# Kernel optimization log

Measured on AMD Instinct MI355X. Metric: run time of the kernel, lower is better.

## Reference

```python
import jax, jax.numpy as jnp
import numpy as np

K = 2  # forward hardcodes k = 2, overriding the k_vector argmax


def setup_inputs() -> dict:
    key = jax.random.key(0)
    k1, k2, k3 = jax.random.split(key, 3)
    points = jax.random.uniform(k1, (4, 8000, 3), dtype=jnp.float32)
    preds = jax.random.uniform(k2, (4, 8000, 256), dtype=jnp.float32)
    k_vector = jax.random.normal(k3, (2,), dtype=jnp.float32)
    return {"points": points, "preds": preds, "k_vector": k_vector}


def reference(points, preds, k_vector):
    # k = argmax(softmax(k_vector)) + 1 is computed then discarded; k = 2.
    # Pairwise euclidean distance (torch.cdist, p=2): [B, N, N]
    sq = jnp.sum(points * points, axis=-1)  # [B, N]
    d2 = sq[:, :, None] + sq[:, None, :] - 2.0 * jnp.einsum(
        'bnd,bmd->bnm', points, points)
    dist = jnp.sqrt(jnp.maximum(d2, 0.0))
    # k smallest distances -> indices of K nearest neighbors (incl. self)
    _, idx = jax.lax.top_k(-dist, K)  # idx: [B, N, K]
    # Gather neighbor features and average: [B, N, K, C] -> [B, N, C]
    knn_preds = jax.vmap(lambda p, i: p[i])(preds, idx)
    return jnp.mean(knn_preds, axis=2)
```

## Files before the change

### kernel.cpp

```cpp
#include <hip/hip_runtime.h>
#include <math.h>

#define BATCH 4
#define NPTS  8000
#define NCH   256
#define GDIM  20
#define NCELL (GDIM*GDIM*GDIM)
#define CELLH (1.0f/GDIM)
#define EPS   1e-5f

#define STRIDE_ST (NCELL + 16)
#define WS_STARTS 0
#define WS_PSORT  131072

__device__ __forceinline__ int cell_clamp(float v) {
  int c = (int)(v * (float)GDIM);
  return c < 0 ? 0 : (c > GDIM - 1 ? GDIM - 1 : c);
}

__global__ __launch_bounds__(1024) void build_kernel(const float* __restrict__ points,
                                                     int* __restrict__ starts,
                                                     float4* __restrict__ psort) {
  __shared__ int lst[NCELL];
  __shared__ int wtot[16];
  const int t = threadIdx.x;
  const int b = blockIdx.x;
  if (t < 1000) {
#pragma unroll
    for (int k = 0; k < 8; ++k) lst[t * 8 + k] = 0;
  }
  __syncthreads();

  const float* pb = points + (size_t)b * NPTS * 3;
  float px[8], py[8], pz[8];
  int pc[8];
  if (t < 1000) {
    const float4* pv = (const float4*)pb;
    const float4 a0 = pv[t * 6 + 0], a1 = pv[t * 6 + 1], a2 = pv[t * 6 + 2];
    const float4 a3 = pv[t * 6 + 3], a4 = pv[t * 6 + 4], a5 = pv[t * 6 + 5];
    px[0] = a0.x; py[0] = a0.y; pz[0] = a0.z;
    px[1] = a0.w; py[1] = a1.x; pz[1] = a1.y;
    px[2] = a1.z; py[2] = a1.w; pz[2] = a2.x;
    px[3] = a2.y; py[3] = a2.z; pz[3] = a2.w;
    px[4] = a3.x; py[4] = a3.y; pz[4] = a3.z;
    px[5] = a3.w; py[5] = a4.x; pz[5] = a4.y;
    px[6] = a4.z; py[6] = a4.w; pz[6] = a5.x;
    px[7] = a5.y; py[7] = a5.z; pz[7] = a5.w;
#pragma unroll
    for (int k = 0; k < 8; ++k) {
      pc[k] = (cell_clamp(pz[k]) * GDIM + cell_clamp(py[k])) * GDIM + cell_clamp(px[k]);
      atomicAdd(&lst[pc[k]], 1);
    }
  }
  __syncthreads();

  int v[8];
  int sum = 0;
  if (t < 1000) {
#pragma unroll
    for (int k = 0; k < 8; ++k) {
      v[k] = lst[t * 8 + k];
      sum += v[k];
    }
  }
  const int lane = t & 63, wv = t >> 6;
  int incl = sum;
#pragma unroll
  for (int d = 1; d < 64; d <<= 1) {
    const int u = __shfl_up(incl, d);
    if (lane >= d) incl += u;
  }
  if (lane == 63) wtot[wv] = incl;
  __syncthreads();
  if (wv == 0) {
    int x = (lane < 16) ? wtot[lane] : 0;
#pragma unroll
    for (int d = 1; d < 16; d <<= 1) {
      const int u = __shfl_up(x, d);
      if (lane >= d) x += u;
    }
    if (lane < 16) wtot[lane] = x;
  }
  __syncthreads();
  const int base = incl - sum + (wv ? wtot[wv - 1] : 0);

  int* stg = starts + b * STRIDE_ST;
  if (t < 1000) {
    int run = base;
#pragma unroll
    for (int k = 0; k < 8; ++k) {
      stg[t * 8 + k] = run;
      lst[t * 8 + k] = run;
      run += v[k];
    }
  }
  if (t == 0) stg[NCELL] = NPTS;
  __syncthreads();

  float4* psb = psort + (size_t)b * NPTS;
  if (t < 1000) {
#pragma unroll
    for (int k = 0; k < 8; ++k) {
      const int pos = atomicAdd(&lst[pc[k]], 1);
      psb[pos] = make_float4(px[k], py[k], pz[k], __int_as_float(t * 8 + k));
    }
  }
}

#define SCAN_RANGE(P0, P1)                                        \
  for (int p = (P0); p < (P1); ++p) {                             \
    const float4 P = ps[p];                                       \
    const float dot = xi * P.x + yi * P.y + zi * P.z;             \
    const float sqj = P.x * P.x + P.y * P.y + P.z * P.z;          \
    const float d2 = fmaxf((sqi + sqj) - 2.0f * dot, 0.0f);       \
    const int j = __float_as_int(P.w);                            \
    const bool lt = (p != i) &&                                   \
        ((d2 < b0) || (d2 == b0 && j < j0));                      \
    b0 = lt ? d2 : b0;                                            \
    j0 = lt ? j : j0;                                             \
  }

#define MERGE_XOR(MASK)                                           \
  {                                                               \
    const float ob = __shfl_xor(mb0, MASK);                       \
    const int oj = __shfl_xor(mj0, MASK);                         \
    const bool keep = (mb0 < ob) || (mb0 == ob && mj0 < oj);      \
    mb0 = keep ? mb0 : ob;                                        \
    mj0 = keep ? mj0 : oj;                                        \
  }

__global__ __launch_bounds__(256, 8) void search_gather_kernel(
    const float4* __restrict__ psort, const int* __restrict__ starts,
    const float* __restrict__ preds, float* __restrict__ out) {
  const int t = threadIdx.x;
  const int b = blockIdx.y;
  const int ql = t >> 4;
  const int s = t & 15;
  const int i = blockIdx.x * 16 + ql;
  const int* stg = starts + b * STRIDE_ST;
  const float4* ps = psort + (size_t)b * NPTS;
  const float4 Q = ps[i];
  const float xi = Q.x, yi = Q.y, zi = Q.z;
  const int qorig = __float_as_int(Q.w);
  const float sqi = xi * xi + yi * yi + zi * zi;
  const int cx = cell_clamp(xi), cy = cell_clamp(yi), cz = cell_clamp(zi);

  float b0 = INFINITY;
  int j0 = -1;

  {
    int lo0 = 0, hi0 = 0, lo1 = 0, hi1 = 0;
    {
      const int c = s;
      const int dz = c / 9 - 1;
      const int rem = c % 9;
      const int z = cz + dz, y = cy + rem / 3 - 1, x = cx + rem % 3 - 1;
      if ((unsigned)z < GDIM && (unsigned)y < GDIM && (unsigned)x < GDIM) {
        const int cid = (z * GDIM + y) * GDIM + x;
        lo0 = stg[cid];
        hi0 = stg[cid + 1];
      }
    }
    if (s < 11) {
      const int c = s + 16;
      const int dz = c / 9 - 1;
      const int rem = c % 9;
      const int z = cz + dz, y = cy + rem / 3 - 1, x = cx + rem % 3 - 1;
      if ((unsigned)z < GDIM && (unsigned)y < GDIM && (unsigned)x < GDIM) {
        const int cid = (z * GDIM + y) * GDIM + x;
        lo1 = stg[cid];
        hi1 = stg[cid + 1];
      }
    }
    SCAN_RANGE(lo0, hi0)
    SCAN_RANGE(lo1, hi1)
  }

  float mb0 = b0;
  int mj0 = j0;
  MERGE_XOR(1) MERGE_XOR(2) MERGE_XOR(4) MERGE_XOR(8)

  if (!(mb0 + EPS <= CELLH * CELLH)) {
    const int x0c = cx > 1 ? cx - 2 : 0;
    const int x1c = cx < GDIM - 2 ? cx + 2 : GDIM - 1;
    int rs[2], re[2];
#pragma unroll
    for (int rr = 0; rr < 2; ++rr) {
      const int kk = s + rr * 16;
      int lo = 0, hi = 0;
      if (kk < 25) {
        const int z = cz + kk / 5 - 2;
        const int y = cy + kk % 5 - 2;
        if ((unsigned)z < GDIM && (unsigned)y < GDIM) {
          const int rowbase = (z * GDIM + y) * GDIM;
          lo = stg[rowbase + x0c];
          hi = stg[rowbase + x1c + 1];
        }
      }
      rs[rr] = lo;
      re[rr] = hi;
    }
#pragma unroll
    for (int rr = 0; rr < 2; ++rr) { SCAN_RANGE(rs[rr], re[rr]) }

    mb0 = b0; mj0 = j0;
    MERGE_XOR(1) MERGE_XOR(2) MERGE_XOR(4) MERGE_XOR(8)

    if (!(mb0 + EPS <= (2.0f * CELLH) * (2.0f * CELLH))) {
      for (int r = 3; r <= GDIM; ++r) {
        const int W = 2 * r + 1;
        for (int idx = s; idx < W * W; idx += 16) {
          const int dz = idx / W - r;
          const int dy = idx % W - r;
          const int z = cz + dz, y = cy + dy;
          if ((unsigned)z >= GDIM || (unsigned)y >= GDIM) continue;
          const int rowbase = (z * GDIM + y) * GDIM;
          if (dz == -r || dz == r || dy == -r || dy == r) {
            const int xl = cx > r ? cx - r : 0;
            const int xh = cx < GDIM - 1 - r ? cx + r : GDIM - 1;
            const int lo = stg[rowbase + xl], hi = stg[rowbase + xh + 1];
            SCAN_RANGE(lo, hi)
          } else {
            if (cx - r >= 0) {
              const int lo = stg[rowbase + cx - r], hi = stg[rowbase + cx - r + 1];
              SCAN_RANGE(lo, hi)
            }
            if (cx + r <= GDIM - 1) {
              const int lo = stg[rowbase + cx + r], hi = stg[rowbase + cx + r + 1];
              SCAN_RANGE(lo, hi)
            }
          }
        }
        mb0 = b0; mj0 = j0;
        MERGE_XOR(1) MERGE_XOR(2) MERGE_XOR(4) MERGE_XOR(8)
        const float rb = (float)r * CELLH;
        if (mb0 + EPS <= rb * rb) break;
      }
    }
  }

  const int lane = t & 63;
  const float* predb = preds + (size_t)b * NPTS * NCH;
  float* outb = out + (size_t)b * NPTS * NCH;
#pragma unroll
  for (int k = 0; k < 4; ++k) {
    const int c = __shfl(mj0, k * 16);
    const int qo = __shfl(qorig, k * 16);
    const float4 va = ((const float4*)(predb + (size_t)qo * NCH))[lane];
    const float4 vc = ((const float4*)(predb + (size_t)c * NCH))[lane];
    float4 r;
    r.x = 0.5f * (va.x + vc.x);
    r.y = 0.5f * (va.y + vc.y);
    r.z = 0.5f * (va.z + vc.z);
    r.w = 0.5f * (va.w + vc.w);
    ((float4*)(outb + (size_t)qo * NCH))[lane] = r;
  }
}

extern "C" void kernel_launch(void* const* d_in, const int* in_sizes, int n_in,
                              void* d_out, int out_size, void* d_ws, size_t ws_size,
                              hipStream_t stream) {
  const float* points = (const float*)d_in[0];
  const float* preds = (const float*)d_in[1];
  float* out = (float*)d_out;

  char* ws = (char*)d_ws;
  int* starts = (int*)(ws + WS_STARTS);
  float4* psort = (float4*)(ws + WS_PSORT);

  build_kernel<<<BATCH, 1024, 0, stream>>>(points, starts, psort);
  search_gather_kernel<<<dim3(NPTS / 16, BATCH), 256, 0, stream>>>(psort, starts, preds, out);
}
```

Baseline: 34.58 us.

## Replace sorted-grid build with fixed-capacity atomic cell buckets plus spill list

Adds a new path that zeroes per-cell counters, then bins every point in parallel into fixed 5-slot cell buckets with atomics. Points that overflow a bucket go to a per-batch spill list that every query scans. This replaces the earlier build, which ran only one 1024-thread block per batch to do a count/scan/scatter, with a grid-wide build meant to remove that serial latency. Queries now run in original point order. The spill list is capped at 512 entries per batch, and points beyond that cap would be dropped silently; the path is used only when the workspace is large enough.

```diff
diff --git a/kernel.cpp b/kernel.cpp
--- a/kernel.cpp
+++ b/kernel.cpp
@@ -9,14 +9,199 @@
 #define CELLH (1.0f/GDIM)
 #define EPS   1e-5f
 
+#define CAPN  5
+#define SPCAP 512
+#define WS2_CNT   0
+#define WS2_SPILL 131072
+#define WS2_PTS   163840
+#define WS2_TOTAL (163840 + (size_t)BATCH * NCELL * CAPN * 16)
+
 #define STRIDE_ST (NCELL + 16)
 #define WS_STARTS 0
 #define WS_PSORT  131072
+#define WS_FB_TOTAL 643072
 
 __device__ __forceinline__ int cell_clamp(float v) {
   int c = (int)(v * (float)GDIM);
   return c < 0 ? 0 : (c > GDIM - 1 ? GDIM - 1 : c);
 }
+
+
+__global__ void zero_cnt_kernel(int* __restrict__ cnt) {
+  const int g = blockIdx.x * 256 + threadIdx.x;
+  if (g < BATCH * NCELL + BATCH) cnt[g] = 0;
+}
+
+__global__ void build_cap_kernel(const float* __restrict__ points,
+                                 int* __restrict__ cnt,
+                                 float4* __restrict__ cell_pts,
+                                 float4* __restrict__ spill) {
+  const int g = blockIdx.x * 256 + threadIdx.x;
+  if (g >= BATCH * NPTS) return;
+  const int b = g / NPTS;
+  const int j = g - b * NPTS;
+  const float* p = points + (size_t)b * NPTS * 3 + (size_t)j * 3;
+  const float x = p[0], y = p[1], z = p[2];
+  const int cid = (cell_clamp(z) * GDIM + cell_clamp(y)) * GDIM + cell_clamp(x);
+  const float4 rec = make_float4(x, y, z, __int_as_float(j));
+  const int pos = atomicAdd(&cnt[b * NCELL + cid], 1);
+  if (pos < CAPN) {
+    cell_pts[((size_t)b * NCELL + cid) * CAPN + pos] = rec;
+  } else {
+    int* spc = cnt + BATCH * NCELL;
+    const int sp = atomicAdd(&spc[b], 1);
+    if (sp < SPCAP) spill[b * SPCAP + sp] = rec;
+  }
+}
+
+#define CAP_CAND(P)                                               \
+  {                                                               \
+    const float dot = xi * (P).x + yi * (P).y + zi * (P).z;       \
+    const float sqj = (P).x * (P).x + (P).y * (P).y + (P).z * (P).z; \
+    const float d2 = fmaxf((sqi + sqj) - 2.0f * dot, 0.0f);       \
+    const int j = __float_as_int((P).w);                          \
+    const bool lt = (j != i) &&                                   \
+        ((d2 < b0) || (d2 == b0 && j < j0));                      \
+    b0 = lt ? d2 : b0;                                            \
+    j0 = lt ? j : j0;                                             \
+  }
+
+#define CAP_SCAN_CELL(CID)                                        \
+  {                                                               \
+    int n = cntb[(CID)];                                          \
+    n = n < CAPN ? n : CAPN;                                      \
+    const float4* base = cpb + (size_t)(CID) * CAPN;              \
+    for (int slot = 0; slot < n; ++slot) {                        \
+      const float4 P = base[slot];                                \
+      CAP_CAND(P)                                                 \
+    }                                                             \
+  }
+
+#define MERGE_XOR(MASK)                                           \
+  {                                                               \
+    const float ob = __shfl_xor(mb0, MASK);                       \
+    const int oj = __shfl_xor(mj0, MASK);                         \
+    const bool keep = (mb0 < ob) || (mb0 == ob && mj0 < oj);      \
+    mb0 = keep ? mb0 : ob;                                        \
+    mj0 = keep ? mj0 : oj;                                        \
+  }
+
+__global__ __launch_bounds__(256, 8) void search_gather_cap_kernel(
+    const float* __restrict__ points, const int* __restrict__ cnt,
+    const float4* __restrict__ cell_pts, const float4* __restrict__ spill,
+    const float* __restrict__ preds, float* __restrict__ out) {
+  const int t = threadIdx.x;
+  const int b = blockIdx.y;
+  const int ql = t >> 4;
+  const int s = t & 15;
+  const int i = blockIdx.x * 16 + ql;
+  const float* pb = points + (size_t)b * NPTS * 3;
+  const float xi = pb[i * 3 + 0];
+  const float yi = pb[i * 3 + 1];
+  const float zi = pb[i * 3 + 2];
+  const float sqi = xi * xi + yi * yi + zi * zi;
+  const int cx = cell_clamp(xi), cy = cell_clamp(yi), cz = cell_clamp(zi);
+  const int* cntb = cnt + b * NCELL;
+  const float4* cpb = cell_pts + (size_t)b * NCELL * CAPN;
+
+  float b0 = INFINITY;
+  int j0 = -1;
+
+  {
+    const int c = s;
+    const int dz = c / 9 - 1;
+    const int rem = c % 9;
+    const int z = cz + dz, y = cy + rem / 3 - 1, x = cx + rem % 3 - 1;
+    if ((unsigned)z < GDIM && (unsigned)y < GDIM && (unsigned)x < GDIM) {
+      const int cid = (z * GDIM + y) * GDIM + x;
+      CAP_SCAN_CELL(cid)
+    }
+  }
+  if (s < 11) {
+    const int c = s + 16;
+    const int dz = c / 9 - 1;
+    const int rem = c % 9;
+    const int z = cz + dz, y = cy + rem / 3 - 1, x = cx + rem % 3 - 1;
+    if ((unsigned)z < GDIM && (unsigned)y < GDIM && (unsigned)x < GDIM) {
+      const int cid = (z * GDIM + y) * GDIM + x;
+      CAP_SCAN_CELL(cid)
+    }
+  }
+  {
+    const int spn = cnt[BATCH * NCELL + b];
+    const float4* spb = spill + b * SPCAP;
+    for (int u = s; u < spn; u += 16) {
+      const float4 P = spb[u];
+      CAP_CAND(P)
+    }
+  }
+
+  float mb0 = b0;
+  int mj0 = j0;
+  MERGE_XOR(1) MERGE_XOR(2) MERGE_XOR(4) MERGE_XOR(8)
+
+  if (!(mb0 + EPS <= CELLH * CELLH)) {
+#pragma unroll
+    for (int k = 0; k < 8; ++k) {
+      const int c = s + k * 16;
+      if (c < 125) {
+        const int dz = c / 25 - 2;
+        const int rem = c % 25;
+        const int z = cz + dz, y = cy + rem / 5 - 2, x = cx + rem % 5 - 2;
+        if ((unsigned)z < GDIM && (unsigned)y < GDIM && (unsigned)x < GDIM) {
+          const int cid = (z * GDIM + y) * GDIM + x;
+          CAP_SCAN_CELL(cid)
+        }
+      }
+    }
+    mb0 = b0; mj0 = j0;
+    MERGE_XOR(1) MERGE_XOR(2) MERGE_XOR(4) MERGE_XOR(8)
+
+    if (!(mb0 + EPS <= (2.0f * CELLH) * (2.0f * CELLH))) {
+      for (int r = 3; r <= GDIM; ++r) {
+        const int W = 2 * r + 1;
+        for (int idx = s; idx < W * W; idx += 16) {
+          const int dz = idx / W - r;
+          const int dy = idx % W - r;
+          const int z = cz + dz, y = cy + dy;
+          if ((unsigned)z >= GDIM || (unsigned)y >= GDIM) continue;
+          const int rowbase = (z * GDIM + y) * GDIM;
+          if (dz == -r || dz == r || dy == -r || dy == r) {
+            const int xl = cx > r ? cx - r : 0;
+            const int xh = cx < GDIM - 1 - r ? cx + r : GDIM - 1;
+            for (int x = xl; x <= xh; ++x) CAP_SCAN_CELL(rowbase + x)
+          } else {
+            if (cx - r >= 0) CAP_SCAN_CELL(rowbase + cx - r)
+            if (cx + r <= GDIM - 1) CAP_SCAN_CELL(rowbase + cx + r)
+          }
+        }
+        mb0 = b0; mj0 = j0;
+        MERGE_XOR(1) MERGE_XOR(2) MERGE_XOR(4) MERGE_XOR(8)
+        const float rb = (float)r * CELLH;
+        if (mb0 + EPS <= rb * rb) break;
+      }
+    }
+  }
+
+  const int wv = t >> 6;
+  const int lane = t & 63;
+  const float* predb = preds + (size_t)b * NPTS * NCH;
+  float* outb = out + (size_t)b * NPTS * NCH;
+#pragma unroll
+  for (int k = 0; k < 4; ++k) {
+    const int c = __shfl(mj0, k * 16);
+    const int qo = blockIdx.x * 16 + wv * 4 + k;
+    const float4 va = ((const float4*)(predb + (size_t)qo * NCH))[lane];
+    const float4 vc = ((const float4*)(predb + (size_t)c * NCH))[lane];
+    float4 r;
+    r.x = 0.5f * (va.x + vc.x);
+    r.y = 0.5f * (va.y + vc.y);
+    r.z = 0.5f * (va.z + vc.z);
+    r.w = 0.5f * (va.w + vc.w);
+    ((float4*)(outb + (size_t)qo * NCH))[lane] = r;
+  }
+}
+
 
 __global__ __launch_bounds__(1024) void build_kernel(const float* __restrict__ points,
                                                      int* __restrict__ starts,
@@ -118,15 +303,6 @@
         ((d2 < b0) || (d2 == b0 && j < j0));                      \
     b0 = lt ? d2 : b0;                                            \
     j0 = lt ? j : j0;                                             \
-  }
-
-#define MERGE_XOR(MASK)                                           \
-  {                                                               \
-    const float ob = __shfl_xor(mb0, MASK);                       \
-    const int oj = __shfl_xor(mj0, MASK);                         \
-    const bool keep = (mb0 < ob) || (mb0 == ob && mj0 < oj);      \
-    mb0 = keep ? mb0 : ob;                                        \
-    mj0 = keep ? mj0 : oj;                                        \
   }
 
 __global__ __launch_bounds__(256, 8) void search_gather_kernel(
@@ -263,11 +439,21 @@
   const float* points = (const float*)d_in[0];
   const float* preds = (const float*)d_in[1];
   float* out = (float*)d_out;
-
   char* ws = (char*)d_ws;
-  int* starts = (int*)(ws + WS_STARTS);
-  float4* psort = (float4*)(ws + WS_PSORT);
-
-  build_kernel<<<BATCH, 1024, 0, stream>>>(points, starts, psort);
-  search_gather_kernel<<<dim3(NPTS / 16, BATCH), 256, 0, stream>>>(psort, starts, preds, out);
-}
+
+  if (ws_size >= WS2_TOTAL) {
+    int* cnt = (int*)(ws + WS2_CNT);
+    float4* spill = (float4*)(ws + WS2_SPILL);
+    float4* cell_pts = (float4*)(ws + WS2_PTS);
+    const int nz = BATCH * NCELL + BATCH;
+    zero_cnt_kernel<<<(nz + 255) / 256, 256, 0, stream>>>(cnt);
+    build_cap_kernel<<<(BATCH * NPTS + 255) / 256, 256, 0, stream>>>(points, cnt, cell_pts, spill);
+    search_gather_cap_kernel<<<dim3(NPTS / 16, BATCH), 256, 0, stream>>>(
+        points, cnt, cell_pts, spill, preds, out);
+  } else {
+    int* starts = (int*)(ws + WS_STARTS);
+    float4* psort = (float4*)(ws + WS_PSORT);
+    build_kernel<<<BATCH, 1024, 0, stream>>>(points, starts, psort);
+    search_gather_kernel<<<dim3(NPTS / 16, BATCH), 256, 0, stream>>>(psort, starts, preds, out);
+  }
+}
```

New measurement: 43.10 us. 1.25x slower.
